# Performance work log

Hardware: AMD Instinct MI355X
Metric: run time of the kernel (lower is better)

The kernel has to match this reference:

```python
import jax, jax.numpy as jnp
from jax import lax
import numpy as np

# ---- dims / neuron params (match init_kwargs) ----
B, T, ENC, HID = 256, 500, 700, 128
TAU_MEM = 20.0      # tauSr == tauRef == tau_mem
THETA = 1.0         # spike_threshold
SCALE_REF = 1.0
WIDTH_GRAD = 1.0    # tauRho (surrogate width)
SCALE_GRAD = 1.0    # scaleRho (surrogate scale)


def alpha_filter(x, tau, mult):
    """Causal convolution along axis 0 with SLAYER's alpha (SRM) kernel
    h[k] = mult * (k/tau) * exp(1 - k/tau), Ts = 1.  Implemented as an exact
    2-state linear recurrence instead of an O(T^2) FIR conv.
    x: (T, ...) -> y: (T, ...)
    """
    d = jnp.exp(-1.0 / tau)          # per-step decay
    c = mult * jnp.exp(1.0) / tau    # h[k] = c * k * d**k

    def step(carry, xt):
        p, q = carry
        qn = d * q + c * d * p       # output at t (h[0] = 0)
        pn = d * p + xt
        return (pn, qn), qn

    z = jnp.zeros_like(x[0])
    _, y = lax.scan(step, (z, z), x)
    return y


def _spike_core(u):
    """SLAYER getSpikes: at each t, membrane = psp + accumulated refractory
    response (alpha kernel with mult = -2*theta*scaleRef, tau = tauRef) of all
    past spikes; emit spike (1/Ts) when membrane >= theta.
    u: (T, B, C) psp values -> (spikes, post-refractory membrane), both (T, B, C).
    """
    d = jnp.exp(-1.0 / TAU_MEM)
    c = (-2.0 * THETA * SCALE_REF) * jnp.exp(1.0) / TAU_MEM

    def step(carry, ut):
        p, q = carry
        qn = d * q + c * d * p       # refractory contribution at t (0 from spike at t)
        u_t = ut + qn                # membrane after refractory subtraction
        s_t = (u_t >= THETA).astype(ut.dtype)
        pn = d * p + s_t
        return (pn, qn), (s_t, u_t)

    z = jnp.zeros_like(u[0])
    _, (s, u_post) = lax.scan(step, (z, z), u)
    return s, u_post


@jax.custom_vjp
def spike(u):
    return _spike_core(u)[0]


def _spike_fwd(u):
    s, u_post = _spike_core(u)
    return s, u_post


def _spike_bwd(u_post, g):
    # SLAYER surrogate: pdf = scaleRho / (tauRho*theta) * exp(-|u - theta| / (tauRho*theta)),
    # evaluated on the refractory-modified membrane; grad does not flow through
    # the refractory recurrence (matches the torch autograd.Function).
    tc = WIDTH_GRAD * THETA
    pdf = (SCALE_GRAD / tc) * jnp.exp(-jnp.abs(u_post - THETA) / tc)
    return (g * pdf,)


spike.defvjp(_spike_fwd, _spike_bwd)


def setup_inputs():
    key = jax.random.key(0)
    k1, k2, k3 = jax.random.split(key, 3)
    # sparse binary input spike trains (B, T, ENC)
    x = (jax.random.uniform(k1, (B, T, ENC)) < 0.05).astype(jnp.float32)
    w1 = jax.random.normal(k2, (HID, ENC), dtype=jnp.float32) * 0.1
    w2 = jax.random.normal(k3, (1, HID), dtype=jnp.float32) * 0.3
    return {"x": x, "w1": w1, "w2": w2}


def reference(x, w1, w2):
    # x: (B, T, ENC) -> time-major (T, B, ENC) for the temporal scans
    xt = jnp.transpose(x, (1, 0, 2))
    h = jnp.einsum('tbc,hc->tbh', xt, w1)        # slayer.dense (bias-free linear per step)
    h = alpha_filter(h, TAU_MEM, 1.0)            # slayer.psp
    s1 = spike(h)                                # slayer.spike (threshold + refractory)
    o = jnp.einsum('tbh,oh->tbo', s1, w2)
    o = alpha_filter(o, TAU_MEM, 1.0)
    s2 = spike(o)
    return jnp.transpose(s2, (1, 0, 2))          # (B, T, 1), matches out2.movedim(-1, 1)
```

## Files before the change

kernel.cpp:

```cpp
#include <hip/hip_runtime.h>

#define BB  256
#define TT  500
#define ENC 700
#define ENC_PAD 704
#define HID 128

__global__ __launch_bounds__(128) void transpose_w1_kernel(const float* __restrict__ w1,
                                                           float* __restrict__ w1t) {
    int c = blockIdx.x;
    int h = threadIdx.x;
    w1t[c * HID + h] = (c < ENC) ? w1[h * ENC + c] : 0.0f;
}

__global__ __launch_bounds__(256) void spmm3_kernel(const float* __restrict__ x,
                                                    const float* __restrict__ w1t,
                                                    float* __restrict__ h) {
    __shared__ ushort lists[4][144];
    const int lane = threadIdx.x & 63;
    const int w = threadIdx.x >> 6;
    const int r = blockIdx.x * 4 + w;
    const float* xrow = x + (size_t)r * ENC;
    const unsigned long long lanemask_lt = (1ull << lane) - 1ull;

    float xv[11];
    #pragma unroll
    for (int k = 0; k < 11; ++k) {
        int c = k * 64 + lane;
        xv[k] = (c < ENC) ? xrow[c] : 0.0f;
    }

    int base = 0;
    #pragma unroll
    for (int k = 0; k < 11; ++k) {
        bool act = (xv[k] != 0.0f);
        unsigned long long m = __ballot(act);
        if (act) {
            int pos = base + (int)__popcll(m & lanemask_lt);
            if (pos < 128) lists[w][pos] = (ushort)(k * 64 + lane);
        }
        base += (int)__popcll(m);
    }
    int n = (base < 128) ? base : 128;
    int npad = (n + 15) & ~15;
    if (lane < npad - n) lists[w][n + lane] = (ushort)ENC;
    __syncthreads();

    float accx = 0.f, accy = 0.f;
    for (int j = 0; j < npad; j += 16) {
        int c0  = lists[w][j +  0], c1  = lists[w][j +  1];
        int c2  = lists[w][j +  2], c3  = lists[w][j +  3];
        int c4  = lists[w][j +  4], c5  = lists[w][j +  5];
        int c6  = lists[w][j +  6], c7  = lists[w][j +  7];
        int c8  = lists[w][j +  8], c9  = lists[w][j +  9];
        int c10 = lists[w][j + 10], c11 = lists[w][j + 11];
        int c12 = lists[w][j + 12], c13 = lists[w][j + 13];
        int c14 = lists[w][j + 14], c15 = lists[w][j + 15];
        float2 t0  = ((const float2*)(w1t + (size_t)c0  * HID))[lane];
        float2 t1  = ((const float2*)(w1t + (size_t)c1  * HID))[lane];
        float2 t2  = ((const float2*)(w1t + (size_t)c2  * HID))[lane];
        float2 t3  = ((const float2*)(w1t + (size_t)c3  * HID))[lane];
        float2 t4  = ((const float2*)(w1t + (size_t)c4  * HID))[lane];
        float2 t5  = ((const float2*)(w1t + (size_t)c5  * HID))[lane];
        float2 t6  = ((const float2*)(w1t + (size_t)c6  * HID))[lane];
        float2 t7  = ((const float2*)(w1t + (size_t)c7  * HID))[lane];
        float2 t8  = ((const float2*)(w1t + (size_t)c8  * HID))[lane];
        float2 t9  = ((const float2*)(w1t + (size_t)c9  * HID))[lane];
        float2 t10 = ((const float2*)(w1t + (size_t)c10 * HID))[lane];
        float2 t11 = ((const float2*)(w1t + (size_t)c11 * HID))[lane];
        float2 t12 = ((const float2*)(w1t + (size_t)c12 * HID))[lane];
        float2 t13 = ((const float2*)(w1t + (size_t)c13 * HID))[lane];
        float2 t14 = ((const float2*)(w1t + (size_t)c14 * HID))[lane];
        float2 t15 = ((const float2*)(w1t + (size_t)c15 * HID))[lane];
        accx += t0.x;  accy += t0.y;
        accx += t1.x;  accy += t1.y;
        accx += t2.x;  accy += t2.y;
        accx += t3.x;  accy += t3.y;
        accx += t4.x;  accy += t4.y;
        accx += t5.x;  accy += t5.y;
        accx += t6.x;  accy += t6.y;
        accx += t7.x;  accy += t7.y;
        accx += t8.x;  accy += t8.y;
        accx += t9.x;  accy += t9.y;
        accx += t10.x; accy += t10.y;
        accx += t11.x; accy += t11.y;
        accx += t12.x; accy += t12.y;
        accx += t13.x; accy += t13.y;
        accx += t14.x; accy += t14.y;
        accx += t15.x; accy += t15.y;
    }

    int b = r / TT;
    int t = r - b * TT;
    float2* dst = (float2*)(h + (size_t)t * (BB * HID) + (size_t)b * HID);
    dst[lane] = make_float2(accx, accy);
}

__device__ __forceinline__ void async_copy4(const float* g, float* l) {
    __builtin_amdgcn_global_load_lds(
        (const __attribute__((address_space(1))) void*)g,
        (__attribute__((address_space(3))) void*)l,
        4, 0, 0);
}

__global__ __launch_bounds__(128) void recur_kernel(const float* __restrict__ hgl,
                                                    const float* __restrict__ w2,
                                                    float* __restrict__ out) {
    __shared__ float hbuf[2][50 * 128];
    __shared__ float vbuf[50 * 129];
    __shared__ float pbuf[2][50];

    const int b = blockIdx.x;
    const int tid = threadIdx.x;
    const int lane = tid & 63;
    const int w = tid >> 6;

    const float D   = 0.95122942450071400910f;
    const float CD  = (float)(0.13591409142295226 * 0.95122942450071400910);
    const float CRD = (float)(-0.27182818284590452 * 0.95122942450071400910);

    float ap = 0.f, aq = 0.f, rp = 0.f, rq = 0.f;
    float Ap = 0.f, Aq = 0.f, Rp = 0.f, Rq = 0.f;
    const float w2v = w2[tid];

    auto stage = [&](int chunk, int buf) {
        const int t0 = chunk * 50 + w * 25;
        #pragma unroll 5
        for (int i = 0; i < 25; ++i) {
            const float* g = hgl + (size_t)(t0 + i) * (BB * HID) + (size_t)b * HID + lane;
            float* l = &hbuf[buf][(w * 25 + i) * 128];
            async_copy4(g, l);
            async_copy4(g + 64, l + 64);
        }
    };

    stage(0, 0);
    __syncthreads();

    for (int chunk = 0; chunk < 10; ++chunk) {
        const int cur = chunk & 1;
        if (chunk < 9) stage(chunk + 1, cur ^ 1);

        const float* hb = &hbuf[cur][0];
        #pragma unroll
        for (int tl = 0; tl < 50; ++tl) {
            float hv = hb[tl * 128 + tid];
            float y = fmaf(D, aq, CD * ap);
            aq = y;
            ap = fmaf(D, ap, hv);
            float q = fmaf(D, rq, CRD * rp);
            float u = y + q;
            float s = (u >= 1.0f) ? 1.0f : 0.0f;
            rq = q;
            rp = fmaf(D, rp, s);
            vbuf[tl * 129 + tid] = s * w2v;
        }
        __syncthreads();

        if (tid < 50) {
            const float* row = &vbuf[tid * 129];
            float a0 = 0.f, a1 = 0.f, a2 = 0.f, a3 = 0.f;
            #pragma unroll
            for (int k = 0; k < 64; k += 4) {
                a0 += row[k]; a1 += row[k + 1]; a2 += row[k + 2]; a3 += row[k + 3];
            }
            pbuf[0][tid] = (a0 + a1) + (a2 + a3);
        } else if (tid >= 64 && tid < 114) {
            const float* row = &vbuf[(tid - 64) * 129 + 64];
            float a0 = 0.f, a1 = 0.f, a2 = 0.f, a3 = 0.f;
            #pragma unroll
            for (int k = 0; k < 64; k += 4) {
                a0 += row[k]; a1 += row[k + 1]; a2 += row[k + 2]; a3 += row[k + 3];
            }
            pbuf[1][tid - 64] = (a0 + a1) + (a2 + a3);
        }
        __syncthreads();

        float my_s2 = 0.f;
        #pragma unroll
        for (int tl = 0; tl < 50; ++tl) {
            float ot = pbuf[0][tl] + pbuf[1][tl];
            float y2 = fmaf(D, Aq, CD * Ap);
            Aq = y2;
            Ap = fmaf(D, Ap, ot);
            float q2 = fmaf(D, Rq, CRD * Rp);
            float u2 = y2 + q2;
            float s2 = (u2 >= 1.0f) ? 1.0f : 0.0f;
            Rq = q2;
            Rp = fmaf(D, Rp, s2);
            if (tl == tid) my_s2 = s2;
        }
        if (tid < 50) out[(size_t)b * TT + chunk * 50 + tid] = my_s2;
    }
}

extern "C" void kernel_launch(void* const* d_in, const int* in_sizes, int n_in,
                              void* d_out, int out_size, void* d_ws, size_t ws_size,
                              hipStream_t stream) {
    const float* x  = (const float*)d_in[0];
    const float* w1 = (const float*)d_in[1];
    const float* w2 = (const float*)d_in[2];
    float* out = (float*)d_out;

    float* h   = (float*)d_ws;
    float* w1t = h + (size_t)TT * BB * HID;

    hipLaunchKernelGGL(transpose_w1_kernel, dim3(ENC_PAD), dim3(HID), 0, stream, w1, w1t);
    hipLaunchKernelGGL(spmm3_kernel, dim3((BB * TT) / 4), dim3(256), 0, stream, x, w1t, h);
    hipLaunchKernelGGL(recur_kernel, dim3(BB), dim3(128), 0, stream, h, w2, out);
}
```

Baseline: 617.5 us.

## Split sparse matmul into compress and LDS-resident w1 gather; register-prefetch recurrence

Splits the sparse x·w1 product into two kernels. The first compacts each row's active input indices into a global list capped at 80 entries. The second keeps a 16-channel slice of transposed w1 in LDS and gathers from there, so it no longer does scattered global reads of w1 rows. The recurrence kernel now prefetches the next chunk into float4 registers instead of using async global-to-LDS copies, with a padded LDS stride. This adds an extra pass that writes and reads the lists, and the lower cap of 80 (down from 128) risks dropping active inputs in rows that have more spikes.

```diff
diff --git a/kernel.cpp b/kernel.cpp
--- a/kernel.cpp
+++ b/kernel.cpp
@@ -5,12 +5,129 @@
 #define ENC 700
 #define ENC_PAD 704
 #define HID 128
+#define LMAX 80
 
 __global__ __launch_bounds__(128) void transpose_w1_kernel(const float* __restrict__ w1,
                                                            float* __restrict__ w1t) {
     int c = blockIdx.x;
     int h = threadIdx.x;
     w1t[c * HID + h] = (c < ENC) ? w1[h * ENC + c] : 0.0f;
+}
+
+__global__ __launch_bounds__(256) void compress_kernel(const float* __restrict__ x,
+                                                       ushort* __restrict__ lists,
+                                                       int* __restrict__ ncnt) {
+    __shared__ ushort lds[4][LMAX];
+    const int lane = threadIdx.x & 63;
+    const int w = threadIdx.x >> 6;
+    const int r = blockIdx.x * 4 + w;
+    const float* xrow = x + (size_t)r * ENC;
+    const unsigned long long lt = (1ull << lane) - 1ull;
+
+    float xv[11];
+    #pragma unroll
+    for (int k = 0; k < 11; ++k) {
+        int c = k * 64 + lane;
+        xv[k] = (c < ENC) ? xrow[c] : 0.0f;
+    }
+    int base = 0;
+    #pragma unroll
+    for (int k = 0; k < 11; ++k) {
+        bool act = (xv[k] != 0.0f);
+        unsigned long long m = __ballot(act);
+        if (act) {
+            int pos = base + (int)__popcll(m & lt);
+            if (pos < LMAX) lds[w][pos] = (ushort)(k * 64 + lane);
+        }
+        base += (int)__popcll(m);
+    }
+    int n = (base < LMAX) ? base : LMAX;
+    for (int p = n + lane; p < LMAX; p += 64) lds[w][p] = (ushort)ENC;
+    if (lane == 0) ncnt[r] = n;
+    if (lane < LMAX / 2)
+        ((uint*)lists)[(size_t)r * (LMAX / 2) + lane] =
+            ((const uint*)lds)[w * (LMAX / 2) + lane];
+}
+
+#define GROWS 512
+#define GRP   64
+#define QCH   16
+#define WST   18
+
+__global__ __launch_bounds__(256) void gather_kernel(const ushort* __restrict__ lists,
+                                                     const int* __restrict__ ncnt,
+                                                     const float* __restrict__ w1t,
+                                                     float* __restrict__ h) {
+    __shared__ float  w1q[ENC_PAD * WST];
+    __shared__ ushort ll[GRP * LMAX];
+    __shared__ int    nb[GRP];
+
+    const int tid = threadIdx.x;
+    const int lane = tid & 63;
+    const int w = tid >> 6;
+    const int q = blockIdx.y;
+    const int r0b = blockIdx.x * GROWS;
+
+    for (int i = tid; i < ENC_PAD * QCH; i += 256) {
+        int c = i >> 4, ch = i & 15;
+        w1q[c * WST + ch] = w1t[c * HID + q * QCH + ch];
+    }
+
+    const int chl = (lane & 7) * 2;
+    const int rw  = lane >> 3;
+
+    for (int g = 0; g < GROWS / GRP; ++g) {
+        const int r0 = r0b + g * GRP;
+        __syncthreads();
+        {
+            const uint* src = (const uint*)lists + (size_t)r0 * (LMAX / 2);
+            uint* dst = (uint*)ll;
+            #pragma unroll
+            for (int k = 0; k < 10; ++k) dst[tid + k * 256] = src[tid + k * 256];
+        }
+        if (tid < GRP) nb[tid] = ncnt[r0 + tid];
+        __syncthreads();
+
+        #pragma unroll
+        for (int p = 0; p < 2; ++p) {
+            const int rl = p * 32 + w * 8 + rw;
+            int n = nb[rl];
+            n = max(n, __shfl_xor(n, 8));
+            n = max(n, __shfl_xor(n, 16));
+            n = max(n, __shfl_xor(n, 32));
+            const int jmax = (n + 7) & ~7;
+
+            float a0 = 0.f, a1 = 0.f;
+            for (int j = 0; j < jmax; j += 8) {
+                uint4 iv = *(const uint4*)&ll[rl * LMAX + j];
+                int c0 = (int)(iv.x & 0xffff), c1 = (int)(iv.x >> 16);
+                int c2 = (int)(iv.y & 0xffff), c3 = (int)(iv.y >> 16);
+                int c4 = (int)(iv.z & 0xffff), c5 = (int)(iv.z >> 16);
+                int c6 = (int)(iv.w & 0xffff), c7 = (int)(iv.w >> 16);
+                float2 v0 = *(const float2*)&w1q[c0 * WST + chl];
+                float2 v1 = *(const float2*)&w1q[c1 * WST + chl];
+                float2 v2 = *(const float2*)&w1q[c2 * WST + chl];
+                float2 v3 = *(const float2*)&w1q[c3 * WST + chl];
+                float2 v4 = *(const float2*)&w1q[c4 * WST + chl];
+                float2 v5 = *(const float2*)&w1q[c5 * WST + chl];
+                float2 v6 = *(const float2*)&w1q[c6 * WST + chl];
+                float2 v7 = *(const float2*)&w1q[c7 * WST + chl];
+                a0 += v0.x; a1 += v0.y;
+                a0 += v1.x; a1 += v1.y;
+                a0 += v2.x; a1 += v2.y;
+                a0 += v3.x; a1 += v3.y;
+                a0 += v4.x; a1 += v4.y;
+                a0 += v5.x; a1 += v5.y;
+                a0 += v6.x; a1 += v6.y;
+                a0 += v7.x; a1 += v7.y;
+            }
+            const int r = r0 + rl;
+            const int b = r / TT;
+            const int t = r - b * TT;
+            *(float2*)&h[(size_t)t * (BB * HID) + (size_t)b * HID + q * QCH + chl] =
+                make_float2(a0, a1);
+        }
+    }
 }
 
 __global__ __launch_bounds__(256) void spmm3_kernel(const float* __restrict__ x,
@@ -21,7 +138,7 @@
     const int w = threadIdx.x >> 6;
     const int r = blockIdx.x * 4 + w;
     const float* xrow = x + (size_t)r * ENC;
-    const unsigned long long lanemask_lt = (1ull << lane) - 1ull;
+    const unsigned long long lt = (1ull << lane) - 1ull;
 
     float xv[11];
     #pragma unroll
@@ -29,14 +146,13 @@
         int c = k * 64 + lane;
         xv[k] = (c < ENC) ? xrow[c] : 0.0f;
     }
-
     int base = 0;
     #pragma unroll
     for (int k = 0; k < 11; ++k) {
         bool act = (xv[k] != 0.0f);
         unsigned long long m = __ballot(act);
         if (act) {
-            int pos = base + (int)__popcll(m & lanemask_lt);
+            int pos = base + (int)__popcll(m & lt);
             if (pos < 128) lists[w][pos] = (ushort)(k * 64 + lane);
         }
         base += (int)__popcll(m);
@@ -48,11 +164,11 @@
 
     float accx = 0.f, accy = 0.f;
     for (int j = 0; j < npad; j += 16) {
-        int c0  = lists[w][j +  0], c1  = lists[w][j +  1];
-        int c2  = lists[w][j +  2], c3  = lists[w][j +  3];
-        int c4  = lists[w][j +  4], c5  = lists[w][j +  5];
-        int c6  = lists[w][j +  6], c7  = lists[w][j +  7];
-        int c8  = lists[w][j +  8], c9  = lists[w][j +  9];
+        int c0  = lists[w][j + 0],  c1  = lists[w][j + 1];
+        int c2  = lists[w][j + 2],  c3  = lists[w][j + 3];
+        int c4  = lists[w][j + 4],  c5  = lists[w][j + 5];
+        int c6  = lists[w][j + 6],  c7  = lists[w][j + 7];
+        int c8  = lists[w][j + 8],  c9  = lists[w][j + 9];
         int c10 = lists[w][j + 10], c11 = lists[w][j + 11];
         int c12 = lists[w][j + 12], c13 = lists[w][j + 13];
         int c14 = lists[w][j + 14], c15 = lists[w][j + 15];
@@ -72,48 +188,30 @@
         float2 t13 = ((const float2*)(w1t + (size_t)c13 * HID))[lane];
         float2 t14 = ((const float2*)(w1t + (size_t)c14 * HID))[lane];
         float2 t15 = ((const float2*)(w1t + (size_t)c15 * HID))[lane];
-        accx += t0.x;  accy += t0.y;
-        accx += t1.x;  accy += t1.y;
-        accx += t2.x;  accy += t2.y;
-        accx += t3.x;  accy += t3.y;
-        accx += t4.x;  accy += t4.y;
-        accx += t5.x;  accy += t5.y;
-        accx += t6.x;  accy += t6.y;
-        accx += t7.x;  accy += t7.y;
-        accx += t8.x;  accy += t8.y;
-        accx += t9.x;  accy += t9.y;
-        accx += t10.x; accy += t10.y;
-        accx += t11.x; accy += t11.y;
-        accx += t12.x; accy += t12.y;
-        accx += t13.x; accy += t13.y;
-        accx += t14.x; accy += t14.y;
-        accx += t15.x; accy += t15.y;
-    }
-
+        accx += t0.x;  accy += t0.y;  accx += t1.x;  accy += t1.y;
+        accx += t2.x;  accy += t2.y;  accx += t3.x;  accy += t3.y;
+        accx += t4.x;  accy += t4.y;  accx += t5.x;  accy += t5.y;
+        accx += t6.x;  accy += t6.y;  accx += t7.x;  accy += t7.y;
+        accx += t8.x;  accy += t8.y;  accx += t9.x;  accy += t9.y;
+        accx += t10.x; accy += t10.y; accx += t11.x; accy += t11.y;
+        accx += t12.x; accy += t12.y; accx += t13.x; accy += t13.y;
+        accx += t14.x; accy += t14.y; accx += t15.x; accy += t15.y;
+    }
     int b = r / TT;
     int t = r - b * TT;
     float2* dst = (float2*)(h + (size_t)t * (BB * HID) + (size_t)b * HID);
     dst[lane] = make_float2(accx, accy);
 }
 
-__device__ __forceinline__ void async_copy4(const float* g, float* l) {
-    __builtin_amdgcn_global_load_lds(
-        (const __attribute__((address_space(1))) void*)g,
-        (__attribute__((address_space(3))) void*)l,
-        4, 0, 0);
-}
-
-__global__ __launch_bounds__(128) void recur_kernel(const float* __restrict__ hgl,
-                                                    const float* __restrict__ w2,
-                                                    float* __restrict__ out) {
-    __shared__ float hbuf[2][50 * 128];
+__global__ __launch_bounds__(128) void recur2_kernel(const float* __restrict__ hgl,
+                                                     const float* __restrict__ w2,
+                                                     float* __restrict__ out) {
+    __shared__ float hbuf[52 * 132];
     __shared__ float vbuf[50 * 129];
     __shared__ float pbuf[2][50];
 
     const int b = blockIdx.x;
     const int tid = threadIdx.x;
-    const int lane = tid & 63;
-    const int w = tid >> 6;
 
     const float D   = 0.95122942450071400910f;
     const float CD  = (float)(0.13591409142295226 * 0.95122942450071400910);
@@ -123,28 +221,36 @@
     float Ap = 0.f, Aq = 0.f, Rp = 0.f, Rq = 0.f;
     const float w2v = w2[tid];
 
-    auto stage = [&](int chunk, int buf) {
-        const int t0 = chunk * 50 + w * 25;
-        #pragma unroll 5
-        for (int i = 0; i < 25; ++i) {
-            const float* g = hgl + (size_t)(t0 + i) * (BB * HID) + (size_t)b * HID + lane;
-            float* l = &hbuf[buf][(w * 25 + i) * 128];
-            async_copy4(g, l);
-            async_copy4(g + 64, l + 64);
-        }
-    };
-
-    stage(0, 0);
-    __syncthreads();
+    const int tl0 = tid >> 5;
+    const int ch0 = (tid & 31) * 4;
+    const float* hb = hgl + (size_t)b * HID + ch0;
+
+    float4 pf[13];
+    #pragma unroll
+    for (int i = 0; i < 13; ++i) {
+        int t = i * 4 + tl0;
+        pf[i] = *(const float4*)(hb + (size_t)t * (BB * HID));
+    }
 
     for (int chunk = 0; chunk < 10; ++chunk) {
-        const int cur = chunk & 1;
-        if (chunk < 9) stage(chunk + 1, cur ^ 1);
-
-        const float* hb = &hbuf[cur][0];
+        #pragma unroll
+        for (int i = 0; i < 13; ++i)
+            *(float4*)&hbuf[(i * 4 + tl0) * 132 + ch0] = pf[i];
+        __syncthreads();
+
+        {
+            const int tb = (chunk + 1) * 50;
+            #pragma unroll
+            for (int i = 0; i < 13; ++i) {
+                int t = tb + i * 4 + tl0;
+                t = (t < TT) ? t : (TT - 1);
+                pf[i] = *(const float4*)(hb + (size_t)t * (BB * HID));
+            }
+        }
+
         #pragma unroll
         for (int tl = 0; tl < 50; ++tl) {
-            float hv = hb[tl * 128 + tid];
+            float hv = hbuf[tl * 132 + tid];
             float y = fmaf(D, aq, CD * ap);
             aq = y;
             ap = fmaf(D, ap, hv);
@@ -202,10 +308,25 @@
     const float* w2 = (const float*)d_in[2];
     float* out = (float*)d_out;
 
+    const size_t H_ELEMS   = (size_t)TT * BB * HID;
+    const size_t W1T_ELEMS = (size_t)ENC_PAD * HID;
     float* h   = (float*)d_ws;
-    float* w1t = h + (size_t)TT * BB * HID;
+    float* w1t = h + H_ELEMS;
+    char* base2 = (char*)(w1t + W1T_ELEMS);
+    ushort* lists = (ushort*)base2;
+    int* ncnt = (int*)(base2 + (size_t)BB * TT * LMAX * 2);
+    const size_t NEED = (size_t)(base2 - (char*)d_ws) +
+                        (size_t)BB * TT * LMAX * 2 + (size_t)BB * TT * 4;
 
     hipLaunchKernelGGL(transpose_w1_kernel, dim3(ENC_PAD), dim3(HID), 0, stream, w1, w1t);
-    hipLaunchKernelGGL(spmm3_kernel, dim3((BB * TT) / 4), dim3(256), 0, stream, x, w1t, h);
-    hipLaunchKernelGGL(recur_kernel, dim3(BB), dim3(128), 0, stream, h, w2, out);
-}
+    if (ws_size >= NEED) {
+        hipLaunchKernelGGL(compress_kernel, dim3((BB * TT) / 4), dim3(256), 0, stream,
+                           x, lists, ncnt);
+        hipLaunchKernelGGL(gather_kernel, dim3(BB * TT / GROWS, HID / QCH), dim3(256),
+                           0, stream, lists, ncnt, w1t, h);
+    } else {
+        hipLaunchKernelGGL(spmm3_kernel, dim3((BB * TT) / 4), dim3(256), 0, stream,
+                           x, w1t, h);
+    }
+    hipLaunchKernelGGL(recur2_kernel, dim3(BB), dim3(128), 0, stream, h, w2, out);
+}
```

Result: slower. 630.5 us (+2.1%).

## Fuse sparse input projection into per-batch recurrence kernel

Applied to the files above, without the earlier changes.

Merges the separate sparse matmul and recurrence kernels into one kernel with one block per batch element. Each block gathers W1 columns for its own timesteps in 50-step chunks into shared memory, then runs the two spiking recurrences on them. This removes the round trip of the large intermediate h tensor through global memory and one kernel launch. The cost is that the input projection now runs on only 256 blocks with four waves each, so x-load latency is much less hidden and the projection is serialized with the recurrence inside every block. The nonzero list cap also drops to 80 entries per row.

```diff
diff --git a/kernel.cpp b/kernel.cpp
--- a/kernel.cpp
+++ b/kernel.cpp
@@ -5,6 +5,7 @@
 #define ENC 700
 #define ENC_PAD 704
 #define HID 128
+#define LMAX 80
 
 __global__ __launch_bounds__(128) void transpose_w1_kernel(const float* __restrict__ w1,
                                                            float* __restrict__ w1t) {
@@ -13,107 +14,69 @@
     w1t[c * HID + h] = (c < ENC) ? w1[h * ENC + c] : 0.0f;
 }
 
-__global__ __launch_bounds__(256) void spmm3_kernel(const float* __restrict__ x,
-                                                    const float* __restrict__ w1t,
-                                                    float* __restrict__ h) {
-    __shared__ ushort lists[4][144];
-    const int lane = threadIdx.x & 63;
-    const int w = threadIdx.x >> 6;
-    const int r = blockIdx.x * 4 + w;
-    const float* xrow = x + (size_t)r * ENC;
-    const unsigned long long lanemask_lt = (1ull << lane) - 1ull;
-
-    float xv[11];
+
+__device__ __forceinline__ void load_xrow(const float* __restrict__ xrow,
+                                          float* xv, int lane) {
     #pragma unroll
     for (int k = 0; k < 11; ++k) {
         int c = k * 64 + lane;
         xv[k] = (c < ENC) ? xrow[c] : 0.0f;
     }
-
+}
+
+__device__ __forceinline__ int compress_row(const float* xv, ushort* list, int lane,
+                                            unsigned long long lt) {
     int base = 0;
     #pragma unroll
     for (int k = 0; k < 11; ++k) {
         bool act = (xv[k] != 0.0f);
         unsigned long long m = __ballot(act);
         if (act) {
-            int pos = base + (int)__popcll(m & lanemask_lt);
-            if (pos < 128) lists[w][pos] = (ushort)(k * 64 + lane);
+            int pos = base + (int)__popcll(m & lt);
+            if (pos < LMAX) list[pos] = (ushort)(k * 64 + lane);
         }
         base += (int)__popcll(m);
     }
-    int n = (base < 128) ? base : 128;
+    int n = (base < LMAX) ? base : LMAX;
     int npad = (n + 15) & ~15;
-    if (lane < npad - n) lists[w][n + lane] = (ushort)ENC;
-    __syncthreads();
-
-    float accx = 0.f, accy = 0.f;
-    for (int j = 0; j < npad; j += 16) {
-        int c0  = lists[w][j +  0], c1  = lists[w][j +  1];
-        int c2  = lists[w][j +  2], c3  = lists[w][j +  3];
-        int c4  = lists[w][j +  4], c5  = lists[w][j +  5];
-        int c6  = lists[w][j +  6], c7  = lists[w][j +  7];
-        int c8  = lists[w][j +  8], c9  = lists[w][j +  9];
-        int c10 = lists[w][j + 10], c11 = lists[w][j + 11];
-        int c12 = lists[w][j + 12], c13 = lists[w][j + 13];
-        int c14 = lists[w][j + 14], c15 = lists[w][j + 15];
-        float2 t0  = ((const float2*)(w1t + (size_t)c0  * HID))[lane];
-        float2 t1  = ((const float2*)(w1t + (size_t)c1  * HID))[lane];
-        float2 t2  = ((const float2*)(w1t + (size_t)c2  * HID))[lane];
-        float2 t3  = ((const float2*)(w1t + (size_t)c3  * HID))[lane];
-        float2 t4  = ((const float2*)(w1t + (size_t)c4  * HID))[lane];
-        float2 t5  = ((const float2*)(w1t + (size_t)c5  * HID))[lane];
-        float2 t6  = ((const float2*)(w1t + (size_t)c6  * HID))[lane];
-        float2 t7  = ((const float2*)(w1t + (size_t)c7  * HID))[lane];
-        float2 t8  = ((const float2*)(w1t + (size_t)c8  * HID))[lane];
-        float2 t9  = ((const float2*)(w1t + (size_t)c9  * HID))[lane];
-        float2 t10 = ((const float2*)(w1t + (size_t)c10 * HID))[lane];
-        float2 t11 = ((const float2*)(w1t + (size_t)c11 * HID))[lane];
-        float2 t12 = ((const float2*)(w1t + (size_t)c12 * HID))[lane];
-        float2 t13 = ((const float2*)(w1t + (size_t)c13 * HID))[lane];
-        float2 t14 = ((const float2*)(w1t + (size_t)c14 * HID))[lane];
-        float2 t15 = ((const float2*)(w1t + (size_t)c15 * HID))[lane];
-        accx += t0.x;  accy += t0.y;
-        accx += t1.x;  accy += t1.y;
-        accx += t2.x;  accy += t2.y;
-        accx += t3.x;  accy += t3.y;
-        accx += t4.x;  accy += t4.y;
-        accx += t5.x;  accy += t5.y;
-        accx += t6.x;  accy += t6.y;
-        accx += t7.x;  accy += t7.y;
-        accx += t8.x;  accy += t8.y;
-        accx += t9.x;  accy += t9.y;
-        accx += t10.x; accy += t10.y;
-        accx += t11.x; accy += t11.y;
-        accx += t12.x; accy += t12.y;
-        accx += t13.x; accy += t13.y;
-        accx += t14.x; accy += t14.y;
-        accx += t15.x; accy += t15.y;
-    }
-
-    int b = r / TT;
-    int t = r - b * TT;
-    float2* dst = (float2*)(h + (size_t)t * (BB * HID) + (size_t)b * HID);
-    dst[lane] = make_float2(accx, accy);
-}
-
-__device__ __forceinline__ void async_copy4(const float* g, float* l) {
-    __builtin_amdgcn_global_load_lds(
-        (const __attribute__((address_space(1))) void*)g,
-        (__attribute__((address_space(3))) void*)l,
-        4, 0, 0);
-}
-
-__global__ __launch_bounds__(128) void recur_kernel(const float* __restrict__ hgl,
-                                                    const float* __restrict__ w2,
-                                                    float* __restrict__ out) {
-    __shared__ float hbuf[2][50 * 128];
+    for (int p = n + lane; p < npad; p += 64) list[p] = (ushort)ENC;
+    return npad;
+}
+
+__device__ __forceinline__ void gather8(const float* __restrict__ wb, uint4 iv,
+                                        float& ax, float& ay) {
+    float2 v0 = *(const float2*)(wb + ((size_t)(iv.x & 0xffffu) << 7));
+    float2 v1 = *(const float2*)(wb + ((size_t)(iv.x >> 16)     << 7));
+    float2 v2 = *(const float2*)(wb + ((size_t)(iv.y & 0xffffu) << 7));
+    float2 v3 = *(const float2*)(wb + ((size_t)(iv.y >> 16)     << 7));
+    float2 v4 = *(const float2*)(wb + ((size_t)(iv.z & 0xffffu) << 7));
+    float2 v5 = *(const float2*)(wb + ((size_t)(iv.z >> 16)     << 7));
+    float2 v6 = *(const float2*)(wb + ((size_t)(iv.w & 0xffffu) << 7));
+    float2 v7 = *(const float2*)(wb + ((size_t)(iv.w >> 16)     << 7));
+    ax += v0.x; ay += v0.y;
+    ax += v1.x; ay += v1.y;
+    ax += v2.x; ay += v2.y;
+    ax += v3.x; ay += v3.y;
+    ax += v4.x; ay += v4.y;
+    ax += v5.x; ay += v5.y;
+    ax += v6.x; ay += v6.y;
+    ax += v7.x; ay += v7.y;
+}
+
+__global__ __launch_bounds__(256, 1) void fused_kernel(const float* __restrict__ x,
+                                                       const float* __restrict__ w1t,
+                                                       const float* __restrict__ w2,
+                                                       float* __restrict__ out) {
+    __shared__ float hch[50 * 132];
     __shared__ float vbuf[50 * 129];
     __shared__ float pbuf[2][50];
+    __shared__ __align__(16) ushort lists[4][2][LMAX];
 
     const int b = blockIdx.x;
     const int tid = threadIdx.x;
     const int lane = tid & 63;
     const int w = tid >> 6;
+    const unsigned long long lt = (1ull << lane) - 1ull;
 
     const float D   = 0.95122942450071400910f;
     const float CD  = (float)(0.13591409142295226 * 0.95122942450071400910);
@@ -121,39 +84,69 @@
 
     float ap = 0.f, aq = 0.f, rp = 0.f, rq = 0.f;
     float Ap = 0.f, Aq = 0.f, Rp = 0.f, Rq = 0.f;
-    const float w2v = w2[tid];
-
-    auto stage = [&](int chunk, int buf) {
-        const int t0 = chunk * 50 + w * 25;
-        #pragma unroll 5
-        for (int i = 0; i < 25; ++i) {
-            const float* g = hgl + (size_t)(t0 + i) * (BB * HID) + (size_t)b * HID + lane;
-            float* l = &hbuf[buf][(w * 25 + i) * 128];
-            async_copy4(g, l);
-            async_copy4(g + 64, l + 64);
-        }
-    };
-
-    stage(0, 0);
-    __syncthreads();
+    const float w2v = (tid < HID) ? w2[tid] : 0.0f;
+
+    const float* wb = w1t + 2 * lane;
+    ushort* l0 = lists[w][0];
+    ushort* l1 = lists[w][1];
 
     for (int chunk = 0; chunk < 10; ++chunk) {
-        const int cur = chunk & 1;
-        if (chunk < 9) stage(chunk + 1, cur ^ 1);
-
-        const float* hb = &hbuf[cur][0];
-        #pragma unroll
-        for (int tl = 0; tl < 50; ++tl) {
-            float hv = hb[tl * 128 + tid];
-            float y = fmaf(D, aq, CD * ap);
-            aq = y;
-            ap = fmaf(D, ap, hv);
-            float q = fmaf(D, rq, CRD * rp);
-            float u = y + q;
-            float s = (u >= 1.0f) ? 1.0f : 0.0f;
-            rq = q;
-            rp = fmaf(D, rp, s);
-            vbuf[tl * 129 + tid] = s * w2v;
+        {
+            const float* xbase = x + ((size_t)b * TT + chunk * 50) * ENC;
+            float xa[11], xb[11], xa2[11], xb2[11];
+            int p = w;
+            if (p < 25) {
+                load_xrow(xbase + (size_t)(2 * p) * ENC, xa, lane);
+                load_xrow(xbase + (size_t)(2 * p + 1) * ENC, xb, lane);
+            }
+            for (; p < 25; p += 4) {
+                int npad0 = compress_row(xa, l0, lane, lt);
+                int npad1 = compress_row(xb, l1, lane, lt);
+                int jmax = (npad0 > npad1) ? npad0 : npad1;
+                for (int q2 = npad0 + lane; q2 < jmax; q2 += 64) l0[q2] = (ushort)ENC;
+                for (int q2 = npad1 + lane; q2 < jmax; q2 += 64) l1[q2] = (ushort)ENC;
+
+                if (p + 4 < 25) {
+                    load_xrow(xbase + (size_t)(2 * (p + 4)) * ENC, xa2, lane);
+                    load_xrow(xbase + (size_t)(2 * (p + 4) + 1) * ENC, xb2, lane);
+                }
+
+                float a0x = 0.f, a0y = 0.f, a1x = 0.f, a1y = 0.f;
+                for (int j = 0; j < jmax; j += 16) {
+                    uint4 ia0 = *(const uint4*)&l0[j];
+                    uint4 ia1 = *(const uint4*)&l0[j + 8];
+                    uint4 ib0 = *(const uint4*)&l1[j];
+                    uint4 ib1 = *(const uint4*)&l1[j + 8];
+                    gather8(wb, ia0, a0x, a0y);
+                    gather8(wb, ia1, a0x, a0y);
+                    gather8(wb, ib0, a1x, a1y);
+                    gather8(wb, ib1, a1x, a1y);
+                }
+                *(float2*)&hch[(2 * p) * 132 + 2 * lane]     = make_float2(a0x, a0y);
+                *(float2*)&hch[(2 * p + 1) * 132 + 2 * lane] = make_float2(a1x, a1y);
+
+                if (p + 4 < 25) {
+                    #pragma unroll
+                    for (int k = 0; k < 11; ++k) { xa[k] = xa2[k]; xb[k] = xb2[k]; }
+                }
+            }
+        }
+        __syncthreads();
+
+        if (tid < HID) {
+            #pragma unroll
+            for (int tl = 0; tl < 50; ++tl) {
+                float hv = hch[tl * 132 + tid];
+                float y = fmaf(D, aq, CD * ap);
+                aq = y;
+                ap = fmaf(D, ap, hv);
+                float q = fmaf(D, rq, CRD * rp);
+                float u = y + q;
+                float s = (u >= 1.0f) ? 1.0f : 0.0f;
+                rq = q;
+                rp = fmaf(D, rp, s);
+                vbuf[tl * 129 + tid] = s * w2v;
+            }
         }
         __syncthreads();
 
@@ -161,16 +154,16 @@
             const float* row = &vbuf[tid * 129];
             float a0 = 0.f, a1 = 0.f, a2 = 0.f, a3 = 0.f;
             #pragma unroll
-            for (int k = 0; k < 64; k += 4) {
-                a0 += row[k]; a1 += row[k + 1]; a2 += row[k + 2]; a3 += row[k + 3];
+            for (int kk = 0; kk < 64; kk += 4) {
+                a0 += row[kk]; a1 += row[kk + 1]; a2 += row[kk + 2]; a3 += row[kk + 3];
             }
             pbuf[0][tid] = (a0 + a1) + (a2 + a3);
         } else if (tid >= 64 && tid < 114) {
             const float* row = &vbuf[(tid - 64) * 129 + 64];
             float a0 = 0.f, a1 = 0.f, a2 = 0.f, a3 = 0.f;
             #pragma unroll
-            for (int k = 0; k < 64; k += 4) {
-                a0 += row[k]; a1 += row[k + 1]; a2 += row[k + 2]; a3 += row[k + 3];
+            for (int kk = 0; kk < 64; kk += 4) {
+                a0 += row[kk]; a1 += row[kk + 1]; a2 += row[kk + 2]; a3 += row[kk + 3];
             }
             pbuf[1][tid - 64] = (a0 + a1) + (a2 + a3);
         }
@@ -202,10 +195,10 @@
     const float* w2 = (const float*)d_in[2];
     float* out = (float*)d_out;
 
-    float* h   = (float*)d_ws;
-    float* w1t = h + (size_t)TT * BB * HID;
-
-    hipLaunchKernelGGL(transpose_w1_kernel, dim3(ENC_PAD), dim3(HID), 0, stream, w1, w1t);
-    hipLaunchKernelGGL(spmm3_kernel, dim3((BB * TT) / 4), dim3(256), 0, stream, x, w1t, h);
-    hipLaunchKernelGGL(recur_kernel, dim3(BB), dim3(128), 0, stream, h, w2, out);
-}
+    float* w1t = (float*)d_ws;
+
+    hipLaunchKernelGGL(transpose_w1_kernel, dim3(ENC_PAD), dim3(HID), 0, stream,
+                       w1, w1t);
+    hipLaunchKernelGGL(fused_kernel, dim3(BB), dim3(256), 0, stream,
+                       x, w1t, w2, out);
+}
```

New measurement: 718.6 us. 16.4% more time.
